# Kernel optimization log

Measured on AMD Instinct MI355X. Metric: run time of the kernel, lower is better.

## Reference

```python
import jax, jax.numpy as jnp
import numpy as np

NUM_GRAPHS = 128
NODES_PER_GRAPH = 512
LATENT_DIM = 256


def setup_inputs() -> dict:
    key = jax.random.key(0)
    n_total = NUM_GRAPHS * NODES_PER_GRAPH
    z = jax.random.normal(key, (n_total, LATENT_DIM), dtype=jnp.float32)
    # sorted graph assignment: nodes of graph i are contiguous
    batch = (jnp.arange(n_total, dtype=jnp.int32) // NODES_PER_GRAPH).astype(jnp.int32)
    return {"z": z, "batch": batch, "num_graphs": NUM_GRAPHS, "max_nodes": NODES_PER_GRAPH}


def reference(z, batch, num_graphs, max_nodes):
    # Eval-mode forward (dropout is identity when not training).
    n_total, d = z.shape
    ones = jnp.ones((n_total,), dtype=jnp.int32)
    counts = jax.ops.segment_sum(ones, batch, num_segments=num_graphs)  # [G]
    starts = jnp.concatenate([jnp.zeros((1,), jnp.int32), jnp.cumsum(counts)[:-1].astype(jnp.int32)])
    pos = jnp.arange(n_total, dtype=jnp.int32) - starts[batch]  # intra-graph node index
    # Scatter nodes into zero-padded [G, max_nodes, D] tensor
    z_pad = jnp.zeros((num_graphs, max_nodes, d), dtype=z.dtype).at[batch, pos].set(z)
    valid = jnp.zeros((num_graphs, max_nodes), dtype=bool).at[batch, pos].set(True)
    # Per-graph inner-product decoder + sigmoid, padded positions forced to 0
    adj = jax.nn.sigmoid(jnp.einsum('gnd,gmd->gnm', z_pad, z_pad))  # [G, N, N]
    mask = valid[:, :, None] & valid[:, None, :]
    return jnp.where(mask, adj, jnp.zeros((), dtype=adj.dtype))
```

## Files before the change

kernel.cpp:

```cpp
#include <hip/hip_runtime.h>

typedef __fp16 fp16x2 __attribute__((ext_vector_type(2)));
typedef _Float16 half8 __attribute__((ext_vector_type(8)));
typedef float floatx4 __attribute__((ext_vector_type(4)));

namespace {

constexpr int NODES = 512;
constexpr int DIM   = 256;
constexpr int BM    = 128;
constexpr int BK    = 64;

union Cvt8 { fp16x2 h2[4]; half8 h8; };

__device__ inline half8 pack8(const float4 f0, const float4 f1) {
  Cvt8 c;
  c.h2[0] = __builtin_amdgcn_cvt_pkrtz(f0.x, f0.y);
  c.h2[1] = __builtin_amdgcn_cvt_pkrtz(f0.z, f0.w);
  c.h2[2] = __builtin_amdgcn_cvt_pkrtz(f1.x, f1.y);
  c.h2[3] = __builtin_amdgcn_cvt_pkrtz(f1.z, f1.w);
  return c.h8;
}

__device__ inline void async_ld16(const void* g, void* lds) {
  __builtin_amdgcn_global_load_lds(
      (const __attribute__((address_space(1))) unsigned int*)g,
      (__attribute__((address_space(3))) unsigned int*)lds,
      16, 0, 0);
}

__global__ __launch_bounds__(256)
void cvt_kernel(const float* __restrict__ z, _Float16* __restrict__ z16) {
  const int i = blockIdx.x * 256 + threadIdx.x;
  const float4* p = reinterpret_cast<const float4*>(z) + (size_t)i * 2;
  const float4 f0 = p[0], f1 = p[1];
  reinterpret_cast<half8*>(z16)[i] = pack8(f0, f1);
}

__global__ __launch_bounds__(256, 4)
void gemm_kernel(const _Float16* __restrict__ z16, float* __restrict__ out) {
  __shared__ __align__(16) _Float16 As[BM * BK];
  __shared__ __align__(16) _Float16 Bs[BM * BK];

  const int bid = blockIdx.x;
  const int g    = (bid & 7) + 8 * (bid >> 7);
  const int tile = (bid >> 3) & 15;
  const int tn   = tile >> 2;
  const int tm   = tile & 3;

  const int tid  = threadIdx.x;
  const int lane = tid & 63;
  const int wave = tid >> 6;
  const int wRow = wave >> 1;
  const int wCol = wave & 1;
  const int lrow = lane & 15;
  const int quad = lane >> 4;

  const _Float16* zA = z16 + ((size_t)g * NODES + tn * BM) * DIM;
  const _Float16* zB = z16 + ((size_t)g * NODES + tm * BM) * DIM;

  const int sRow = lane >> 3;
  const int sCp  = (lane & 7) ^ sRow;
  const size_t sOffH = (size_t)sRow * DIM + sCp * 8;

  floatx4 acc[4][4];
#pragma unroll
  for (int i = 0; i < 4; ++i)
#pragma unroll
    for (int j = 0; j < 4; ++j)
      acc[i][j] = (floatx4){0.f, 0.f, 0.f, 0.f};

  for (int kk = 0; kk < DIM; kk += BK) {
#pragma unroll
    for (int it = 0; it < 4; ++it) {
      const int q = wave * 4 + it;
      const _Float16* gA = zA + (size_t)q * 8 * DIM + kk + sOffH;
      const _Float16* gB = zB + (size_t)q * 8 * DIM + kk + sOffH;
      async_ld16(gA, &As[q * 512]);
      async_ld16(gB, &Bs[q * 512]);
    }
    __syncthreads();

#pragma unroll
    for (int ks = 0; ks < 2; ++ks) {
      half8 af[4], bf[4];
#pragma unroll
      for (int i = 0; i < 4; ++i) {
        const int row = wRow * 64 + i * 16 + lrow;
        const int cp = (ks * 4 + quad) ^ (lrow & 7);
        af[i] = *reinterpret_cast<const half8*>(&As[row * BK + cp * 8]);
      }
#pragma unroll
      for (int j = 0; j < 4; ++j) {
        const int row = wCol * 64 + j * 16 + lrow;
        const int cp = (ks * 4 + quad) ^ (lrow & 7);
        bf[j] = *reinterpret_cast<const half8*>(&Bs[row * BK + cp * 8]);
      }
#pragma unroll
      for (int i = 0; i < 4; ++i)
#pragma unroll
        for (int j = 0; j < 4; ++j)
          acc[i][j] = __builtin_amdgcn_mfma_f32_16x16x32_f16(af[i], bf[j], acc[i][j], 0, 0, 0);
    }
    __syncthreads();
  }

  float* outg = out + (size_t)g * NODES * NODES;
  const int nBase = tn * BM + wRow * 64;
  const int mBase = tm * BM + wCol * 64;
#pragma unroll
  for (int i = 0; i < 4; ++i) {
#pragma unroll
    for (int j = 0; j < 4; ++j) {
      const int m = mBase + j * 16 + lrow;
#pragma unroll
      for (int r = 0; r < 4; ++r) {
        const int n = nBase + i * 16 + quad * 4 + r;
        const float x = acc[i][j][r];
        outg[(size_t)n * NODES + m] = __builtin_amdgcn_rcpf(1.0f + __expf(-x));
      }
    }
  }
}

constexpr int LSTR = 72;
__global__ __launch_bounds__(256, 4)
void fallback_kernel(const float* __restrict__ z, float* __restrict__ out) {
  __shared__ _Float16 As[BM * LSTR];
  __shared__ _Float16 Bs[BM * LSTR];
  const int bid = blockIdx.x;
  const int g    = (bid & 7) + 8 * (bid >> 7);
  const int tile = (bid >> 3) & 15;
  const int tn   = tile >> 2;
  const int tm   = tile & 3;
  const int tid  = threadIdx.x;
  const int lane = tid & 63;
  const int wave = tid >> 6;
  const int wRow = wave >> 1;
  const int wCol = wave & 1;
  const int lrow = lane & 15;
  const int quad = lane >> 4;
  const float* zA = z + ((size_t)g * NODES + tn * BM) * DIM;
  const float* zB = z + ((size_t)g * NODES + tm * BM) * DIM;
  const int srow  = tid >> 1;
  const int shalf = tid & 1;
  floatx4 acc[4][4];
#pragma unroll
  for (int i = 0; i < 4; ++i)
#pragma unroll
    for (int j = 0; j < 4; ++j)
      acc[i][j] = (floatx4){0.f, 0.f, 0.f, 0.f};
  for (int kk = 0; kk < DIM; kk += BK) {
    {
      const float4* pa = reinterpret_cast<const float4*>(zA + srow * DIM + kk + shalf * 32);
      _Float16* da = &As[srow * LSTR + shalf * 32];
      float4 f0 = pa[0], f1 = pa[1], f2 = pa[2], f3 = pa[3];
      *reinterpret_cast<half8*>(da)     = pack8(f0, f1);
      *reinterpret_cast<half8*>(da + 8) = pack8(f2, f3);
      f0 = pa[4]; f1 = pa[5]; f2 = pa[6]; f3 = pa[7];
      *reinterpret_cast<half8*>(da + 16) = pack8(f0, f1);
      *reinterpret_cast<half8*>(da + 24) = pack8(f2, f3);
    }
    {
      const float4* pb = reinterpret_cast<const float4*>(zB + srow * DIM + kk + shalf * 32);
      _Float16* db = &Bs[srow * LSTR + shalf * 32];
      float4 f0 = pb[0], f1 = pb[1], f2 = pb[2], f3 = pb[3];
      *reinterpret_cast<half8*>(db)     = pack8(f0, f1);
      *reinterpret_cast<half8*>(db + 8) = pack8(f2, f3);
      f0 = pb[4]; f1 = pb[5]; f2 = pb[6]; f3 = pb[7];
      *reinterpret_cast<half8*>(db + 16) = pack8(f0, f1);
      *reinterpret_cast<half8*>(db + 24) = pack8(f2, f3);
    }
    __syncthreads();
#pragma unroll
    for (int ks = 0; ks < 2; ++ks) {
      half8 af[4], bf[4];
#pragma unroll
      for (int i = 0; i < 4; ++i)
        af[i] = *reinterpret_cast<const half8*>(
            &As[(wRow * 64 + i * 16 + lrow) * LSTR + ks * 32 + quad * 8]);
#pragma unroll
      for (int j = 0; j < 4; ++j)
        bf[j] = *reinterpret_cast<const half8*>(
            &Bs[(wCol * 64 + j * 16 + lrow) * LSTR + ks * 32 + quad * 8]);
#pragma unroll
      for (int i = 0; i < 4; ++i)
#pragma unroll
        for (int j = 0; j < 4; ++j)
          acc[i][j] = __builtin_amdgcn_mfma_f32_16x16x32_f16(af[i], bf[j], acc[i][j], 0, 0, 0);
    }
    __syncthreads();
  }
  float* outg = out + (size_t)g * NODES * NODES;
  const int nBase = tn * BM + wRow * 64;
  const int mBase = tm * BM + wCol * 64;
#pragma unroll
  for (int i = 0; i < 4; ++i) {
#pragma unroll
    for (int j = 0; j < 4; ++j) {
      const int m = mBase + j * 16 + lrow;
#pragma unroll
      for (int r = 0; r < 4; ++r) {
        const int n = nBase + i * 16 + quad * 4 + r;
        const float x = acc[i][j][r];
        outg[(size_t)n * NODES + m] = __builtin_amdgcn_rcpf(1.0f + __expf(-x));
      }
    }
  }
}

}

extern "C" void kernel_launch(void* const* d_in, const int* in_sizes, int n_in,
                              void* d_out, int out_size, void* d_ws, size_t ws_size,
                              hipStream_t stream) {
  const float* z = (const float*)d_in[0];
  float* out = (float*)d_out;
  const size_t need = (size_t)128 * 512 * 256 * sizeof(_Float16);
  if (ws_size >= need) {
    _Float16* z16 = (_Float16*)d_ws;
    hipLaunchKernelGGL(cvt_kernel, dim3(8192), dim3(256), 0, stream, z, z16);
    hipLaunchKernelGGL(gemm_kernel, dim3(128 * 16), dim3(256), 0, stream, z16, out);
  } else {
    hipLaunchKernelGGL(fallback_kernel, dim3(128 * 16), dim3(256), 0, stream, z, out);
  }
}
```

Baseline: 217.3 us.

## Store output transposed as float4 nontemporal writes and reorder conversion blocks

The epilogue relies on the output being symmetric (adj[n][m] == adj[m][n]). It writes the tile transposed, so each lane emits contiguous float4 nontemporal stores instead of scalar strided stores. The conversion kernel now uses nontemporal loads and a block ordering that matches the GEMM's graph interleaving, intended to keep freshly converted fp16 data cache-friendly. This relies on exact symmetry of the computed product, which holds because A and B tiles come from the same data with the same summation order.

```diff
diff --git a/kernel.cpp b/kernel.cpp
--- a/kernel.cpp
+++ b/kernel.cpp
@@ -12,6 +12,15 @@
 constexpr int BK    = 64;
 
 union Cvt8 { fp16x2 h2[4]; half8 h8; };
+
+__device__ inline half8 pack8(const floatx4 f0, const floatx4 f1) {
+  Cvt8 c;
+  c.h2[0] = __builtin_amdgcn_cvt_pkrtz(f0.x, f0.y);
+  c.h2[1] = __builtin_amdgcn_cvt_pkrtz(f0.z, f0.w);
+  c.h2[2] = __builtin_amdgcn_cvt_pkrtz(f1.x, f1.y);
+  c.h2[3] = __builtin_amdgcn_cvt_pkrtz(f1.z, f1.w);
+  return c.h8;
+}
 
 __device__ inline half8 pack8(const float4 f0, const float4 f1) {
   Cvt8 c;
@@ -31,10 +40,17 @@
 
 __global__ __launch_bounds__(256)
 void cvt_kernel(const float* __restrict__ z, _Float16* __restrict__ z16) {
-  const int i = blockIdx.x * 256 + threadIdx.x;
-  const float4* p = reinterpret_cast<const float4*>(z) + (size_t)i * 2;
-  const float4 f0 = p[0], f1 = p[1];
-  reinterpret_cast<half8*>(z16)[i] = pack8(f0, f1);
+  const int b = blockIdx.x;
+  const int x = b & 7;
+  const int j = b >> 3;
+  const int g = x + 8 * (j >> 6);
+  const int chunk = j & 63;
+  const size_t base = ((size_t)g * NODES + (size_t)chunk * 8) * DIM
+                    + (size_t)threadIdx.x * 8;
+  const floatx4* p = reinterpret_cast<const floatx4*>(z + base);
+  const floatx4 f0 = __builtin_nontemporal_load(p);
+  const floatx4 f1 = __builtin_nontemporal_load(p + 1);
+  *reinterpret_cast<half8*>(z16 + base) = pack8(f0, f1);
 }
 
 __global__ __launch_bounds__(256, 4)
@@ -109,16 +125,19 @@
   const int nBase = tn * BM + wRow * 64;
   const int mBase = tm * BM + wCol * 64;
 #pragma unroll
-  for (int i = 0; i < 4; ++i) {
-#pragma unroll
-    for (int j = 0; j < 4; ++j) {
-      const int m = mBase + j * 16 + lrow;
+  for (int j = 0; j < 4; ++j) {
+    const int m = mBase + j * 16 + lrow;
+    float* rowp = outg + (size_t)m * NODES;
+#pragma unroll
+    for (int i = 0; i < 4; ++i) {
+      const int n0 = nBase + i * 16 + quad * 4;
+      floatx4 v;
 #pragma unroll
       for (int r = 0; r < 4; ++r) {
-        const int n = nBase + i * 16 + quad * 4 + r;
         const float x = acc[i][j][r];
-        outg[(size_t)n * NODES + m] = __builtin_amdgcn_rcpf(1.0f + __expf(-x));
-      }
+        v[r] = __builtin_amdgcn_rcpf(1.0f + __expf(-x));
+      }
+      __builtin_nontemporal_store(v, reinterpret_cast<floatx4*>(rowp + n0));
     }
   }
 }
@@ -195,16 +214,19 @@
   const int nBase = tn * BM + wRow * 64;
   const int mBase = tm * BM + wCol * 64;
 #pragma unroll
-  for (int i = 0; i < 4; ++i) {
-#pragma unroll
-    for (int j = 0; j < 4; ++j) {
-      const int m = mBase + j * 16 + lrow;
+  for (int j = 0; j < 4; ++j) {
+    const int m = mBase + j * 16 + lrow;
+    float* rowp = outg + (size_t)m * NODES;
+#pragma unroll
+    for (int i = 0; i < 4; ++i) {
+      const int n0 = nBase + i * 16 + quad * 4;
+      floatx4 v;
 #pragma unroll
       for (int r = 0; r < 4; ++r) {
-        const int n = nBase + i * 16 + quad * 4 + r;
         const float x = acc[i][j][r];
-        outg[(size_t)n * NODES + m] = __builtin_amdgcn_rcpf(1.0f + __expf(-x));
-      }
+        v[r] = __builtin_amdgcn_rcpf(1.0f + __expf(-x));
+      }
+      __builtin_nontemporal_store(v, reinterpret_cast<floatx4*>(rowp + n0));
     }
   }
 }
```

Measured after the change: 232.2 us. +6.8%, slower.
